# Performance work log

Measured on AMD Instinct MI355X. Metric: run time of the kernel, lower is better.

## Reference

```python
import jax, jax.numpy as jnp
import numpy as np

B, S, D, H = 2, 512, 1024, 16
HD = D // H
F, E, K = 4096, 8, 2
TEMP = 1.0
EPS = 1e-6


def setup_inputs() -> dict:
    key = jax.random.key(0)
    ks = jax.random.split(key, 12)
    sc = 0.02
    n = lambda k, shp: (jax.random.normal(k, shp, jnp.float32) * sc)
    return {
        "x": jax.random.normal(ks[0], (B, S, D), jnp.float32),
        "norm1_w": jnp.ones((D,), jnp.float32),
        "norm2_w": jnp.ones((D,), jnp.float32),
        "wq": n(ks[1], (D, D)), "bq": jnp.zeros((D,), jnp.float32),
        "wk": n(ks[2], (D, D)), "bk": jnp.zeros((D,), jnp.float32),
        "wv": n(ks[3], (D, D)), "bv": jnp.zeros((D,), jnp.float32),
        "wo": n(ks[4], (D, D)), "bo": jnp.zeros((D,), jnp.float32),
        "wr": n(ks[5], (D, E)), "br": jnp.zeros((E,), jnp.float32),
        "w1": n(ks[6], (E, D, F)), "b1": jnp.zeros((E, F), jnp.float32),
        "w2": n(ks[7], (E, F, D)), "b2": jnp.zeros((E, D), jnp.float32),
    }


def _rmsnorm(x, w):
    return x * jax.lax.rsqrt(jnp.mean(x * x, axis=-1, keepdims=True) + EPS) * w


def reference(x, norm1_w, norm2_w, wq, bq, wk, bk, wv, bv, wo, bo,
              wr, br, w1, b1, w2, b2):
    # ---- pre-norm causal multi-head attention ----
    h = _rmsnorm(x, norm1_w)
    q = (h @ wq + bq).reshape(B, S, H, HD)
    k = (h @ wk + bk).reshape(B, S, H, HD)
    v = (h @ wv + bv).reshape(B, S, H, HD)
    scores = jnp.einsum("bqhd,bkhd->bhqk", q, k) / jnp.sqrt(jnp.float32(HD))
    causal = jnp.tril(jnp.ones((S, S), bool))
    scores = jnp.where(causal, scores, jnp.finfo(scores.dtype).min)
    attn = jax.nn.softmax(scores, axis=-1)
    ctx = jnp.einsum("bhqk,bkhd->bqhd", attn, v).reshape(B, S, D)
    x = x + (ctx @ wo + bo)  # residual (dropout inert, p=0)

    # ---- temperature-scaled top-k MoE FFN ----
    h2 = _rmsnorm(x, norm2_w)
    logits = h2 @ wr + br                         # [B,S,E]
    probs = jax.nn.softmax(logits / TEMP, axis=-1)
    top_p, top_i = jax.lax.top_k(probs, K)        # [B,S,K]
    top_p = top_p / jnp.sum(top_p, axis=-1, keepdims=True)
    onehot = jax.nn.one_hot(top_i, E, dtype=probs.dtype)  # [B,S,K,E]
    combine = jnp.einsum("bsk,bske->bse", top_p, onehot)  # sparse combine weights

    # dense grouped-expert compute (reference form of dispatch/compute/combine)
    hid = jax.nn.silu(jnp.einsum("bsd,edf->bsef", h2, w1) + b1)
    expert_out = jnp.einsum("bsef,efd->bsed", hid, w2) + b2
    ff = jnp.einsum("bse,bsed->bsd", combine, expert_out)

    # load-balancing auxiliary loss: E * sum_i frac_i * mean_prob_i
    frac = jnp.mean(jnp.sum(onehot, axis=2), axis=(0, 1)) / K  # [E]
    mean_prob = jnp.mean(probs, axis=(0, 1))                   # [E]
    aux_loss = jnp.float32(E) * jnp.sum(frac * mean_prob)

    x = x + ff
    return x, aux_loss
```

## Files before the change

### kernel.cpp

```cpp
#include <hip/hip_runtime.h>
#include <math.h>

#define CB 2
#define CS 512
#define CD 1024
#define CH 16
#define CHD 64
#define CF 4096
#define CE 8
#define CK 2
#define CT (CB*CS)
#define CBH (CB*CH)
#define CEPS 1e-6f
#define QKVP 3072
#define MAXROWS 3072
#define MAXTILES (MAXROWS/128)

typedef __attribute__((ext_vector_type(8))) short bf16x8;
typedef __attribute__((ext_vector_type(4))) float f32x4;

__device__ __forceinline__ short f2bf(float f) {
  unsigned u = __float_as_uint(f);
  unsigned r = (u + 0x7FFF + ((u >> 16) & 1)) >> 16;
  return (short)r;
}
__device__ __forceinline__ float bf2f(short h) {
  return __uint_as_float(((unsigned)(unsigned short)h) << 16);
}

__device__ __forceinline__ void gload_lds16(const void* g, void* l) {
  __builtin_amdgcn_global_load_lds(
      (const __attribute__((address_space(1))) unsigned int*)g,
      (__attribute__((address_space(3))) unsigned int*)l, 16, 0, 0);
}

__global__ __launch_bounds__(256) void rmsnorm_hl_kernel(
    const float* __restrict__ x, const float* __restrict__ w,
    short* __restrict__ outH, short* __restrict__ outL) {
  int t = blockIdx.x;
  int tid = threadIdx.x;
  float4 xv = ((const float4*)(x + (size_t)t * CD))[tid];
  float ss = xv.x*xv.x + xv.y*xv.y + xv.z*xv.z + xv.w*xv.w;
  for (int off = 32; off > 0; off >>= 1) ss += __shfl_down(ss, off);
  __shared__ float red[4];
  __shared__ float s_scale;
  int lane = tid & 63, wid = tid >> 6;
  if (lane == 0) red[wid] = ss;
  __syncthreads();
  if (tid == 0) {
    float tot = red[0] + red[1] + red[2] + red[3];
    s_scale = rsqrtf(tot / (float)CD + CEPS);
  }
  __syncthreads();
  float sc = s_scale;
  float4 wv = ((const float4*)w)[tid];
  float o[4] = {xv.x * sc * wv.x, xv.y * sc * wv.y,
                xv.z * sc * wv.z, xv.w * sc * wv.w};
  short4 hi, lo;
  short* hp = (short*)&hi; short* lp = (short*)&lo;
#pragma unroll
  for (int i = 0; i < 4; ++i) {
    short h = f2bf(o[i]);
    hp[i] = h;
    lp[i] = f2bf(o[i] - bf2f(h));
  }
  ((short4*)(outH + (size_t)t * CD))[tid] = hi;
  ((short4*)(outL + (size_t)t * CD))[tid] = lo;
}

__global__ __launch_bounds__(256) void transpose_convert_kernel(
    const float* __restrict__ W, short* __restrict__ Wth,
    short* __restrict__ Wtl, int Kd, int Nd) {
  int e = blockIdx.z;
  const float* Wb = W + (size_t)e * Kd * Nd;
  size_t obase = (size_t)e * Kd * Nd;
  int n0 = blockIdx.x * 64, k0 = blockIdx.y * 64;
  __shared__ float t[64][65];
  int tid = threadIdx.x;
#pragma unroll
  for (int i = 0; i < 4; ++i) {
    int idx = i * 256 + tid;
    int r = idx >> 4, c4 = (idx & 15) * 4;
    float4 v = *(const float4*)(Wb + (size_t)(k0 + r) * Nd + n0 + c4);
    t[r][c4] = v.x; t[r][c4 + 1] = v.y; t[r][c4 + 2] = v.z; t[r][c4 + 3] = v.w;
  }
  __syncthreads();
  int n = tid >> 2, k16 = (tid & 3) * 16;
  short th[16], tl[16];
#pragma unroll
  for (int j = 0; j < 16; ++j) {
    float v = t[k16 + j][n];
    short hi = f2bf(v);
    th[j] = hi;
    tl[j] = f2bf(v - bf2f(hi));
  }
  size_t oo = obase + (size_t)(n0 + n) * Kd + k0 + k16;
  ((int4*)(Wth + oo))[0] = ((int4*)th)[0];
  ((int4*)(Wth + oo + 8))[0] = ((int4*)th)[1];
  if (Wtl) {
    ((int4*)(Wtl + oo))[0] = ((int4*)tl)[0];
    ((int4*)(Wtl + oo + 8))[0] = ((int4*)tl)[1];
  }
}

struct TPtrs {
  const float* w[4];
  short* hh[4];
  short* ll[4];
};
__global__ __launch_bounds__(256) void transpose4_kernel(TPtrs p) {
  int z = blockIdx.z;
  const float* Wb = p.w[z];
  short* Wth = p.hh[z];
  short* Wtl = p.ll[z];
  int n0 = blockIdx.x * 64, k0 = blockIdx.y * 64;
  __shared__ float t[64][65];
  int tid = threadIdx.x;
#pragma unroll
  for (int i = 0; i < 4; ++i) {
    int idx = i * 256 + tid;
    int r = idx >> 4, c4 = (idx & 15) * 4;
    float4 v = *(const float4*)(Wb + (size_t)(k0 + r) * CD + n0 + c4);
    t[r][c4] = v.x; t[r][c4 + 1] = v.y; t[r][c4 + 2] = v.z; t[r][c4 + 3] = v.w;
  }
  __syncthreads();
  int n = tid >> 2, k16 = (tid & 3) * 16;
  short th[16], tl[16];
#pragma unroll
  for (int j = 0; j < 16; ++j) {
    float v = t[k16 + j][n];
    short hi = f2bf(v);
    th[j] = hi;
    tl[j] = f2bf(v - bf2f(hi));
  }
  size_t oo = (size_t)(n0 + n) * CD + k0 + k16;
  ((int4*)(Wth + oo))[0] = ((int4*)th)[0];
  ((int4*)(Wth + oo + 8))[0] = ((int4*)th)[1];
  ((int4*)(Wtl + oo))[0] = ((int4*)tl)[0];
  ((int4*)(Wtl + oo + 8))[0] = ((int4*)tl)[1];
}

__global__ void pack_bias_kernel(const float* __restrict__ bq,
                                 const float* __restrict__ bk,
                                 const float* __restrict__ bv,
                                 float* __restrict__ out) {
  int i = blockIdx.x * 256 + threadIdx.x;
  if (i < QKVP)
    out[i] = (i < 1024) ? bq[i] : (i < 2048 ? bk[i - 1024] : bv[i - 2048]);
}

template <int SILU, int OUTBF>
__global__ __launch_bounds__(512) void moe_gemm_kernel(
    const short* __restrict__ A, const short* __restrict__ Bt,
    const float* __restrict__ bias, void* __restrict__ Cout,
    float* __restrict__ part, int partM, int N, int K,
    const int* __restrict__ tile_e, const int* __restrict__ total_rows) {
  __shared__ __align__(16) short A0[128 * 64], A1[128 * 64];
  __shared__ __align__(16) short B0[256 * 64], B1[256 * 64];
  int tid = threadIdx.x;
  int m0 = blockIdx.y * 128, n0 = blockIdx.x * 256;
  if (m0 >= *total_rows) return;
  int e = tile_e[blockIdx.y];
  const short* Bb = Bt + (size_t)e * N * K;
  const float* biasb = bias ? bias + (size_t)e * N : nullptr;
  int kz = blockIdx.z;
  int kchunk = K / gridDim.z;
  int kbeg = kz * kchunk;
  int nsteps = kchunk >> 6;
  int lane = tid & 63, w = tid >> 6;
  int wr = w >> 2, wc = w & 3;
  int l15 = lane & 15, l4 = lane >> 4;
  f32x4 acc[4][4] = {};

#define STAGE(AS_, BS_, KK)                                                   \
  {                                                                           \
    _Pragma("unroll") for (int i = 0; i < 2; ++i) {                           \
      int c = i * 512 + tid;                                                  \
      int r = c >> 3, gs = c & 7;                                             \
      int g = gs ^ (r & 7);                                                   \
      gload_lds16(A + (size_t)(m0 + r) * K + (KK) + g * 8, &AS_[c * 8]);      \
    }                                                                         \
    _Pragma("unroll") for (int i = 0; i < 4; ++i) {                           \
      int c = i * 512 + tid;                                                  \
      int r = c >> 3, gs = c & 7;                                             \
      int g = gs ^ (r & 7);                                                   \
      gload_lds16(Bb + (size_t)(n0 + r) * K + (KK) + g * 8, &BS_[c * 8]);     \
    }                                                                         \
  }

#define COMPUTE(AS_, BS_)                                                     \
  {                                                                           \
    _Pragma("unroll") for (int ks = 0; ks < 2; ++ks) {                        \
      bf16x8 a[4], b[4];                                                      \
      _Pragma("unroll") for (int m = 0; m < 4; ++m) {                         \
        int row = wr * 64 + m * 16 + l15;                                     \
        int slot = (ks * 4 + l4) ^ (row & 7);                                 \
        a[m] = *(const bf16x8*)&AS_[(row * 8 + slot) * 8];                    \
      }                                                                       \
      _Pragma("unroll") for (int n = 0; n < 4; ++n) {                         \
        int row = wc * 64 + n * 16 + l15;                                     \
        int slot = (ks * 4 + l4) ^ (row & 7);                                 \
        b[n] = *(const bf16x8*)&BS_[(row * 8 + slot) * 8];                    \
      }                                                                       \
      _Pragma("unroll") for (int m = 0; m < 4; ++m)                           \
      _Pragma("unroll") for (int n = 0; n < 4; ++n)                           \
        acc[m][n] = __builtin_amdgcn_mfma_f32_16x16x32_bf16(a[m], b[n],       \
                                                            acc[m][n], 0, 0, 0); \
    }                                                                         \
  }

  STAGE(A0, B0, kbeg);
  __syncthreads();
  for (int s = 0; s < nsteps; s += 2) {
    int k0 = kbeg + (s << 6);
    bool has1 = (s + 1 < nsteps), has2 = (s + 2 < nsteps);
    if (has1) STAGE(A1, B1, k0 + 64);
    COMPUTE(A0, B0);
    __syncthreads();
    if (has1) {
      if (has2) STAGE(A0, B0, k0 + 128);
      COMPUTE(A1, B1);
      __syncthreads();
    }
  }
#undef STAGE
#undef COMPUTE

  if (gridDim.z > 1) {
#pragma unroll
    for (int m = 0; m < 4; ++m) {
      int row = m0 + wr * 64 + m * 16 + l4 * 4;
#pragma unroll
      for (int n = 0; n < 4; ++n) {
        int col = n0 + wc * 64 + n * 16 + l15;
#pragma unroll
        for (int q = 0; q < 4; ++q)
          part[((size_t)kz * partM + row + q) * N + col] = acc[m][n][q];
      }
    }
    return;
  }
  float* outf = (float*)Cout;
  short* outb = (short*)Cout;
#pragma unroll
  for (int m = 0; m < 4; ++m) {
    int row = m0 + wr * 64 + m * 16 + l4 * 4;
#pragma unroll
    for (int n = 0; n < 4; ++n) {
      int col = n0 + wc * 64 + n * 16 + l15;
      float bv = biasb[col];
#pragma unroll
      for (int q = 0; q < 4; ++q) {
        float v = acc[m][n][q] + bv;
        if (SILU) v = v / (1.f + __expf(-v));
        if (OUTBF) outb[(size_t)(row + q) * N + col] = f2bf(v);
        else outf[(size_t)(row + q) * N + col] = v;
      }
    }
  }
}

template <int LO>
__global__ __launch_bounds__(256) void mfma_gemm_kernel(
    const short* __restrict__ Ah, const short* __restrict__ Al,
    const short* __restrict__ Bh, const short* __restrict__ Bl,
    float* __restrict__ part, int partM, int N, int K) {
  __shared__ short As0[4096], Bs0[4096], As1[4096], Bs1[4096];
  __shared__ short Als0[LO ? 4096 : 64], Bls0[LO ? 4096 : 64];
  __shared__ short Als1[LO ? 4096 : 64], Bls1[LO ? 4096 : 64];
  int tid = threadIdx.x;
  int m0 = blockIdx.y * 128, n0 = blockIdx.x * 128;
  int kz = blockIdx.z;
  int kchunk = K / gridDim.z;
  int kbeg = kz * kchunk;
  int nsteps = kchunk >> 5;
  int lane = tid & 63, w = tid >> 6;
  int wr = w >> 1, wc = w & 1;
  int l15 = lane & 15, l4 = lane >> 4;
  int xorl = (l15 & 3) ^ ((l15 >> 2) & 3);
  f32x4 acc[4][4] = {};
  bf16x8 vA0[2], vB0[2], vAl0[2], vBl0[2];
  bf16x8 vA1[2], vB1[2], vAl1[2], vBl1[2];

#define LOAD_SET(VA, VB, VAL, VBL, KK)                                        \
  {                                                                           \
    _Pragma("unroll") for (int ic = 0; ic < 2; ++ic) {                        \
      int c = ic * 256 + tid;                                                 \
      int r = c >> 2, g = c & 3;                                              \
      size_t ao = (size_t)(m0 + r) * K + (KK) + g * 8;                        \
      size_t bo = (size_t)(n0 + r) * K + (KK) + g * 8;                        \
      VA[ic] = *(const bf16x8*)(Ah + ao);                                     \
      VB[ic] = *(const bf16x8*)(Bh + bo);                                     \
      if (LO) {                                                               \
        VAL[ic] = *(const bf16x8*)(Al + ao);                                  \
        VBL[ic] = *(const bf16x8*)(Bl + bo);                                  \
      }                                                                       \
    }                                                                         \
  }

#define WRITE_SET(AS_, BS_, ALS_, BLS_, VA, VB, VAL, VBL)                     \
  {                                                                           \
    _Pragma("unroll") for (int ic = 0; ic < 2; ++ic) {                        \
      int c = ic * 256 + tid;                                                 \
      int r = c >> 2, g = c & 3;                                              \
      int ch = (r * 4 + (g ^ (r & 3) ^ ((r >> 2) & 3))) * 8;                  \
      *(bf16x8*)&AS_[ch] = VA[ic];                                            \
      *(bf16x8*)&BS_[ch] = VB[ic];                                            \
      if (LO) {                                                               \
        *(bf16x8*)&ALS_[ch] = VAL[ic];                                        \
        *(bf16x8*)&BLS_[ch] = VBL[ic];                                        \
      }                                                                       \
    }                                                                         \
  }

#define COMPUTE_SET(AS_, BS_, ALS_, BLS_)                                     \
  {                                                                           \
    bf16x8 ah[4], al[4];                                                      \
    _Pragma("unroll") for (int m = 0; m < 4; ++m) {                           \
      int row = wr * 64 + m * 16 + l15;                                       \
      int idx = (row * 4 + (l4 ^ xorl)) * 8;                                  \
      ah[m] = *(const bf16x8*)&AS_[idx];                                      \
      if (LO) al[m] = *(const bf16x8*)&ALS_[idx];                             \
    }                                                                         \
    _Pragma("unroll") for (int n = 0; n < 4; ++n) {                           \
      int row = wc * 64 + n * 16 + l15;                                       \
      int idx = (row * 4 + (l4 ^ xorl)) * 8;                                  \
      bf16x8 bhn = *(const bf16x8*)&BS_[idx];                                 \
      bf16x8 bln;                                                             \
      if (LO) bln = *(const bf16x8*)&BLS_[idx];                               \
      _Pragma("unroll") for (int m = 0; m < 4; ++m) {                         \
        acc[m][n] = __builtin_amdgcn_mfma_f32_16x16x32_bf16(ah[m], bhn,       \
                                                            acc[m][n], 0, 0, 0); \
        if (LO) {                                                             \
          acc[m][n] = __builtin_amdgcn_mfma_f32_16x16x32_bf16(al[m], bhn,     \
                                                              acc[m][n], 0, 0, 0); \
          acc[m][n] = __builtin_amdgcn_mfma_f32_16x16x32_bf16(ah[m], bln,     \
                                                              acc[m][n], 0, 0, 0); \
        }                                                                     \
      }                                                                       \
    }                                                                         \
  }

  LOAD_SET(vA0, vB0, vAl0, vBl0, kbeg);
  WRITE_SET(As0, Bs0, Als0, Bls0, vA0, vB0, vAl0, vBl0);
  __syncthreads();
  for (int s = 0; s < nsteps; s += 2) {
    int k0 = kbeg + (s << 5);
    bool has1 = (s + 1 < nsteps), has2 = (s + 2 < nsteps);
    if (has1) LOAD_SET(vA1, vB1, vAl1, vBl1, k0 + 32);
    COMPUTE_SET(As0, Bs0, Als0, Bls0);
    if (has1) WRITE_SET(As1, Bs1, Als1, Bls1, vA1, vB1, vAl1, vBl1);
    __syncthreads();
    if (has1) {
      if (has2) LOAD_SET(vA0, vB0, vAl0, vBl0, k0 + 64);
      COMPUTE_SET(As1, Bs1, Als1, Bls1);
      if (has2) WRITE_SET(As0, Bs0, Als0, Bls0, vA0, vB0, vAl0, vBl0);
      __syncthreads();
    }
  }
#undef LOAD_SET
#undef WRITE_SET
#undef COMPUTE_SET

#pragma unroll
  for (int m = 0; m < 4; ++m) {
    int row = m0 + wr * 64 + m * 16 + l4 * 4;
#pragma unroll
    for (int n = 0; n < 4; ++n) {
      int col = n0 + wc * 64 + n * 16 + l15;
#pragma unroll
      for (int q = 0; q < 4; ++q)
        part[((size_t)kz * partM + row + q) * N + col] = acc[m][n][q];
    }
  }
}

__global__ __launch_bounds__(256) void reduce_splitk_kernel(
    const float* __restrict__ part, int partM, int nz,
    const float* __restrict__ bias, float* __restrict__ outp, int N) {
  int row = blockIdx.x;
  for (int c = threadIdx.x * 4; c < N; c += 1024) {
    float4 s = *(const float4*)(part + (size_t)row * N + c);
    for (int z = 1; z < nz; ++z) {
      float4 p = *(const float4*)(part + ((size_t)z * partM + row) * N + c);
      s.x += p.x; s.y += p.y; s.z += p.z; s.w += p.w;
    }
    s.x += bias[c]; s.y += bias[c + 1]; s.z += bias[c + 2]; s.w += bias[c + 3];
    *(float4*)(outp + (size_t)row * N + c) = s;
  }
}

__global__ __launch_bounds__(256) void attn_epilogue_kernel(
    const float* __restrict__ part, const float* __restrict__ bo,
    const float* __restrict__ x, const float* __restrict__ n2w,
    const float* __restrict__ wr, const float* __restrict__ br,
    float* __restrict__ x1, float* __restrict__ h2, int* __restrict__ top_i,
    float* __restrict__ top_p, float* __restrict__ probs_out) {
  int t = blockIdx.x;
  int tid = threadIdx.x;
  int c = tid * 4;
  float4 s = *(const float4*)(part + (size_t)t * CD + c);
#pragma unroll
  for (int z = 1; z < 4; ++z) {
    float4 p = *(const float4*)(part + ((size_t)z * CT + t) * CD + c);
    s.x += p.x; s.y += p.y; s.z += p.z; s.w += p.w;
  }
  float4 bv = *(const float4*)(bo + c);
  float4 xv = *(const float4*)(x + (size_t)t * CD + c);
  s.x += bv.x + xv.x; s.y += bv.y + xv.y;
  s.z += bv.z + xv.z; s.w += bv.w + xv.w;
  *(float4*)(x1 + (size_t)t * CD + c) = s;
  float ss = s.x*s.x + s.y*s.y + s.z*s.z + s.w*s.w;
  for (int off = 32; off > 0; off >>= 1) ss += __shfl_down(ss, off);
  __shared__ float red[4];
  __shared__ float s_scale;
  int lane = tid & 63, wid = tid >> 6;
  if (lane == 0) red[wid] = ss;
  __syncthreads();
  if (tid == 0) {
    float tot = red[0] + red[1] + red[2] + red[3];
    s_scale = rsqrtf(tot / (float)CD + CEPS);
  }
  __syncthreads();
  float sc = s_scale;
  float4 wv = *(const float4*)(n2w + c);
  float hv[4] = {s.x * sc * wv.x, s.y * sc * wv.y,
                 s.z * sc * wv.z, s.w * sc * wv.w};
  *(float4*)(h2 + (size_t)t * CD + c) =
      make_float4(hv[0], hv[1], hv[2], hv[3]);
  float a[CE] = {};
#pragma unroll
  for (int j = 0; j < 4; ++j) {
    const float* wrow = wr + (size_t)(c + j) * CE;
#pragma unroll
    for (int e = 0; e < CE; ++e) a[e] += hv[j] * wrow[e];
  }
  __shared__ float red8[256][CE];
#pragma unroll
  for (int e = 0; e < CE; ++e) red8[tid][e] = a[e];
  __syncthreads();
  for (int st = 128; st > 0; st >>= 1) {
    if (tid < st) {
#pragma unroll
      for (int e = 0; e < CE; ++e) red8[tid][e] += red8[tid + st][e];
    }
    __syncthreads();
  }
  if (tid == 0) {
    float probs[CE];
    float mx = -1e30f;
#pragma unroll
    for (int e = 0; e < CE; ++e) {
      probs[e] = red8[0][e] + br[e];
      mx = fmaxf(mx, probs[e]);
    }
    float sum = 0.f;
#pragma unroll
    for (int e = 0; e < CE; ++e) { probs[e] = __expf(probs[e] - mx); sum += probs[e]; }
    float inv = 1.0f / sum;
#pragma unroll
    for (int e = 0; e < CE; ++e) {
      probs[e] *= inv;
      probs_out[t * CE + e] = probs[e];
    }
    int i1 = 0;
#pragma unroll
    for (int e = 1; e < CE; ++e) if (probs[e] > probs[i1]) i1 = e;
    int i2 = (i1 == 0) ? 1 : 0;
#pragma unroll
    for (int e = 0; e < CE; ++e)
      if (e != i1 && probs[e] > probs[i2]) i2 = e;
    float p1 = probs[i1], p2 = probs[i2];
    float s12 = p1 + p2;
    top_i[t * 2 + 0] = i1;
    top_i[t * 2 + 1] = i2;
    top_p[t * 2 + 0] = p1 / s12;
    top_p[t * 2 + 1] = p2 / s12;
  }
}

__global__ __launch_bounds__(256) void fused_attn_kernel(
    const float* __restrict__ qkv, short* __restrict__ ctxh,
    short* __restrict__ ctxl) {
  __shared__ float Qs[32][68];
  __shared__ float KVs[64 * 68];
  __shared__ float Pt[32][66];
  int qt = blockIdx.x, bh = blockIdx.y;
  int b = bh / CH, h = bh % CH;
  int qrow0 = qt * 32;
  int ktmax = (qrow0 + 31) >> 6;
  int tid = threadIdx.x;
  int cg = tid & 31, rg = tid >> 5;
  int r0 = rg * 4;

#pragma unroll
  for (int it = 0; it < 2; ++it) {
    int idx = it * 256 + tid;
    int r = idx >> 4, c4 = (idx & 15) * 4;
    *(float4*)&Qs[r][c4] = *(const float4*)(
        qkv + (size_t)(b * CS + qrow0 + r) * QKVP + h * CHD + c4);
  }

  float m_i[4], l_i[4], O[4][2];
#pragma unroll
  for (int i = 0; i < 4; ++i) {
    m_i[i] = -1e30f;
    l_i[i] = 0.f;
    O[i][0] = 0.f;
    O[i][1] = 0.f;
  }

  for (int kt = 0; kt <= ktmax; ++kt) {
    __syncthreads();
#pragma unroll
    for (int it = 0; it < 4; ++it) {
      int idx = it * 256 + tid;
      int r = idx >> 4, c4 = (idx & 15) * 4;
      const float* src =
          qkv + (size_t)(b * CS + kt * 64 + r) * QKVP + h * CHD;
      float4 kv = *(const float4*)(src + 1024 + c4);
      KVs[r * 65 + c4 + 0] = kv.x;
      KVs[r * 65 + c4 + 1] = kv.y;
      KVs[r * 65 + c4 + 2] = kv.z;
      KVs[r * 65 + c4 + 3] = kv.w;
    }
    __syncthreads();

    float s[4][2] = {};
#pragma unroll 4
    for (int d = 0; d < 64; ++d) {
      float q0 = Qs[r0 + 0][d];
      float q1 = Qs[r0 + 1][d];
      float q2 = Qs[r0 + 2][d];
      float q3 = Qs[r0 + 3][d];
      float k0 = KVs[(cg * 2 + 0) * 65 + d];
      float k1 = KVs[(cg * 2 + 1) * 65 + d];
      s[0][0] += q0 * k0; s[0][1] += q0 * k1;
      s[1][0] += q1 * k0; s[1][1] += q1 * k1;
      s[2][0] += q2 * k0; s[2][1] += q2 * k1;
      s[3][0] += q3 * k0; s[3][1] += q3 * k1;
    }

#pragma unroll
    for (int i = 0; i < 4; ++i) {
      int gr = qrow0 + r0 + i;
      int gc0 = kt * 64 + cg * 2;
      float s0 = (gc0 + 0 > gr) ? -1e30f : s[i][0] * 0.125f;
      float s1 = (gc0 + 1 > gr) ? -1e30f : s[i][1] * 0.125f;
      float tmax = fmaxf(s0, s1);
#pragma unroll
      for (int off = 16; off > 0; off >>= 1)
        tmax = fmaxf(tmax, __shfl_xor(tmax, off));
      float newm = fmaxf(m_i[i], tmax);
      float p0 = __expf(s0 - newm);
      float p1 = __expf(s1 - newm);
      float tsum = p0 + p1;
#pragma unroll
      for (int off = 16; off > 0; off >>= 1) tsum += __shfl_xor(tsum, off);
      float scale = __expf(m_i[i] - newm);
      l_i[i] = l_i[i] * scale + tsum;
      m_i[i] = newm;
      O[i][0] *= scale;
      O[i][1] *= scale;
      Pt[r0 + i][cg * 2 + 0] = p0;
      Pt[r0 + i][cg * 2 + 1] = p1;
    }
    __syncthreads();

#pragma unroll
    for (int it = 0; it < 4; ++it) {
      int idx = it * 256 + tid;
      int r = idx >> 4, c4 = (idx & 15) * 4;
      *(float4*)&KVs[r * 68 + c4] = *(const float4*)(
          qkv + (size_t)(b * CS + kt * 64 + r) * QKVP + 2048 + h * CHD + c4);
    }
    __syncthreads();

#pragma unroll 4
    for (int c = 0; c < 64; ++c) {
      float p0 = Pt[r0 + 0][c];
      float p1 = Pt[r0 + 1][c];
      float p2 = Pt[r0 + 2][c];
      float p3 = Pt[r0 + 3][c];
      float v0 = KVs[c * 68 + cg];
      float v1 = KVs[c * 68 + cg + 32];
      O[0][0] += p0 * v0; O[0][1] += p0 * v1;
      O[1][0] += p1 * v0; O[1][1] += p1 * v1;
      O[2][0] += p2 * v0; O[2][1] += p2 * v1;
      O[3][0] += p3 * v0; O[3][1] += p3 * v1;
    }
  }

#pragma unroll
  for (int i = 0; i < 4; ++i) {
    float inv = 1.0f / l_i[i];
#pragma unroll
    for (int jd = 0; jd < 2; ++jd) {
      int dv = cg + 32 * jd;
      size_t oi = (size_t)(b * CS + qrow0 + r0 + i) * CD + h * CHD + dv;
      float v = O[i][jd] * inv;
      short hi = f2bf(v);
      ctxh[oi] = hi;
      ctxl[oi] = f2bf(v - bf2f(hi));
    }
  }
}

__global__ __launch_bounds__(256) void finalize_kernel(
    const int* __restrict__ top_i, const float* __restrict__ probs,
    int* __restrict__ offs, int* __restrict__ tile_e,
    int* __restrict__ total_padded, int* __restrict__ row_map,
    int* __restrict__ cursor, float* __restrict__ aux_out) {
  int tid = threadIdx.x;
  __shared__ float redp[256][CE];
  __shared__ int redc[256][CE];
  float lp[CE] = {};
  int lc[CE] = {};
  for (int t = tid; t < CT; t += 256) {
    lc[top_i[t * 2 + 0]]++;
    lc[top_i[t * 2 + 1]]++;
#pragma unroll
    for (int e = 0; e < CE; ++e) lp[e] += probs[t * CE + e];
  }
#pragma unroll
  for (int e = 0; e < CE; ++e) { redp[tid][e] = lp[e]; redc[tid][e] = lc[e]; }
  __syncthreads();
  for (int s = 128; s > 0; s >>= 1) {
    if (tid < s) {
#pragma unroll
      for (int e = 0; e < CE; ++e) {
        redp[tid][e] += redp[tid + s][e];
        redc[tid][e] += redc[tid + s][e];
      }
    }
    __syncthreads();
  }
  __shared__ int s_off[CE + 1];
  if (tid == 0) {
    int o = 0;
    for (int e = 0; e < CE; ++e) {
      s_off[e] = o;
      offs[e] = o;
      o += ((redc[0][e] + 127) >> 7) << 7;
    }
    s_off[CE] = o;
    offs[CE] = o;
    *total_padded = o;
    int nt = o >> 7;
    for (int i = 0; i < nt; ++i) {
      int e = 0;
      while (e < CE - 1 && i * 128 >= s_off[e + 1]) e++;
      tile_e[i] = e;
    }
    float aux = 0.f;
    for (int e = 0; e < CE; ++e)
      aux += ((float)redc[0][e] / (float)(CT * CK)) * (redp[0][e] / (float)CT);
    aux_out[0] = aux * (float)CE;
  }
  if (tid < CE) cursor[tid] = 0;
  __syncthreads();
  for (int i = tid; i < MAXROWS; i += blockDim.x) row_map[i] = -1;
}

__global__ void gather_kernel(const int* __restrict__ top_i,
                              const int* __restrict__ offs,
                              int* __restrict__ cursor, int* __restrict__ row_map,
                              int* __restrict__ row_of) {
  int idx = blockIdx.x * blockDim.x + threadIdx.x;
  if (idx >= CT * CK) return;
  int e = top_i[idx];
  int pos = offs[e] + atomicAdd(&cursor[e], 1);
  row_map[pos] = idx >> 1;
  row_of[idx] = pos;
}

__global__ __launch_bounds__(256) void gatherx_kernel(
    const float* __restrict__ h2, const int* __restrict__ row_map,
    short* __restrict__ Xg) {
  int row = blockIdx.x;
  int tid = threadIdx.x;
  int tok = row_map[row];
  short4 o;
  if (tok < 0) {
    o = make_short4(0, 0, 0, 0);
  } else {
    float4 v = ((const float4*)(h2 + (size_t)tok * CD))[tid];
    o = make_short4(f2bf(v.x), f2bf(v.y), f2bf(v.z), f2bf(v.w));
  }
  ((short4*)(Xg + (size_t)row * CD))[tid] = o;
}

__global__ __launch_bounds__(256) void combine_g2_kernel(
    const float* __restrict__ part, int partM, int nz,
    const float* __restrict__ b2, const int* __restrict__ tile_e,
    const int* __restrict__ row_of, const float* __restrict__ top_p,
    const float* __restrict__ x1, float* __restrict__ out) {
  int t = blockIdx.x;
  int c = threadIdx.x * 4;
  float4 r = *(const float4*)(x1 + (size_t)t * CD + c);
#pragma unroll
  for (int s = 0; s < CK; ++s) {
    int row = row_of[t * 2 + s];
    int e = tile_e[row >> 7];
    float w = top_p[t * 2 + s];
    float4 acc = *(const float4*)(part + (size_t)row * CD + c);
    for (int z = 1; z < nz; ++z) {
      float4 p = *(const float4*)(part + ((size_t)z * partM + row) * CD + c);
      acc.x += p.x; acc.y += p.y; acc.z += p.z; acc.w += p.w;
    }
    float4 bv = *(const float4*)(b2 + (size_t)e * CD + c);
    r.x += w * (acc.x + bv.x);
    r.y += w * (acc.y + bv.y);
    r.z += w * (acc.z + bv.z);
    r.w += w * (acc.w + bv.w);
  }
  *(float4*)(out + (size_t)t * CD + c) = r;
}

extern "C" void kernel_launch(void* const* d_in, const int* in_sizes, int n_in,
                              void* d_out, int out_size, void* d_ws,
                              size_t ws_size, hipStream_t stream) {
  const float* x   = (const float*)d_in[0];
  const float* n1w = (const float*)d_in[1];
  const float* n2w = (const float*)d_in[2];
  const float* wq  = (const float*)d_in[3];
  const float* bq  = (const float*)d_in[4];
  const float* wk  = (const float*)d_in[5];
  const float* bk  = (const float*)d_in[6];
  const float* wv  = (const float*)d_in[7];
  const float* bv  = (const float*)d_in[8];
  const float* wo  = (const float*)d_in[9];
  const float* bo  = (const float*)d_in[10];
  const float* wr  = (const float*)d_in[11];
  const float* br  = (const float*)d_in[12];
  const float* w1  = (const float*)d_in[13];
  const float* b1  = (const float*)d_in[14];
  const float* w2  = (const float*)d_in[15];
  const float* b2  = (const float*)d_in[16];
  float* out = (float*)d_out;

  char* base = (char*)d_ws;
  size_t off = 0;
  auto alloc = [&](size_t bytes) -> void* {
    void* p = base + off;
    off += (bytes + 255) & ~(size_t)255;
    return p;
  };
  float* f_x1   = (float*)alloc((size_t)CT * CD * 4);
  float* f_h2   = (float*)alloc((size_t)CT * CD * 4);
  short* f_xg   = (short*)alloc((size_t)MAXROWS * CD * 2);
  short* f_hid  = (short*)alloc((size_t)MAXROWS * CF * 2);
  short* f_hh   = (short*)alloc((size_t)CT * CD * 2);
  short* f_hl   = (short*)alloc((size_t)CT * CD * 2);
  short* f_wqkvh = (short*)alloc((size_t)QKVP * CD * 2);
  short* f_wqkvl = (short*)alloc((size_t)QKVP * CD * 2);
  float* f_qkv  = (float*)alloc((size_t)CT * QKVP * 4);
  short* f_ctxh = (short*)alloc((size_t)CT * CD * 2);
  short* f_ctxl = (short*)alloc((size_t)CT * CD * 2);
  short* f_woth = (short*)alloc((size_t)CD * CD * 2);
  short* f_wotl = (short*)alloc((size_t)CD * CD * 2);
  float* f_bqkv = (float*)alloc(QKVP * 4);
  float* f_topp = (float*)alloc(CT * CK * 4);
  float* f_probs = (float*)alloc(CT * CE * 4);
  int* i_topi   = (int*)alloc(CT * CK * 4);
  int* i_rowof  = (int*)alloc(CT * CK * 4);
  int* i_rowmap = (int*)alloc(MAXROWS * 4);
  int* i_cursor = (int*)alloc(CE * 4);
  int* i_offs   = (int*)alloc((CE + 1) * 4);
  int* i_tile   = (int*)alloc(MAXTILES * 4);
  int* i_total  = (int*)alloc(4);
  short* f_wG = (short*)alloc((size_t)CE * CD * CF * 2);
  short* f_w1t = f_wG;
  short* f_w2t = f_wG;
  void* Rs = alloc((size_t)4 * MAXROWS * CD * 4);
  float* f_partqkv = (float*)Rs;
  float* f_partwo = (float*)Rs;
  float* f_partg2 = (float*)Rs;

  dim3 b256(256);

  pack_bias_kernel<<<QKVP / 256, b256, 0, stream>>>(bq, bk, bv, f_bqkv);
  TPtrs tp;
  tp.w[0] = wq; tp.w[1] = wk; tp.w[2] = wv; tp.w[3] = wo;
  tp.hh[0] = f_wqkvh + 0 * (size_t)CD * CD;
  tp.hh[1] = f_wqkvh + 1 * (size_t)CD * CD;
  tp.hh[2] = f_wqkvh + 2 * (size_t)CD * CD;
  tp.hh[3] = f_woth;
  tp.ll[0] = f_wqkvl + 0 * (size_t)CD * CD;
  tp.ll[1] = f_wqkvl + 1 * (size_t)CD * CD;
  tp.ll[2] = f_wqkvl + 2 * (size_t)CD * CD;
  tp.ll[3] = f_wotl;
  transpose4_kernel<<<dim3(16, 16, 4), b256, 0, stream>>>(tp);
  transpose_convert_kernel<<<dim3(CF / 64, CD / 64, CE), b256, 0, stream>>>(
      w1, f_w1t, nullptr, CD, CF);

  rmsnorm_hl_kernel<<<CT, b256, 0, stream>>>(x, n1w, f_hh, f_hl);
  mfma_gemm_kernel<1><<<dim3(QKVP / 128, CT / 128, 2), b256, 0, stream>>>(
      f_hh, f_hl, f_wqkvh, f_wqkvl, f_partqkv, CT, QKVP, CD);
  reduce_splitk_kernel<<<CT, b256, 0, stream>>>(f_partqkv, CT, 2, f_bqkv,
                                                f_qkv, QKVP);
  fused_attn_kernel<<<dim3(CS / 32, CBH), b256, 0, stream>>>(f_qkv, f_ctxh,
                                                             f_ctxl);
  mfma_gemm_kernel<1><<<dim3(CD / 128, CT / 128, 4), b256, 0, stream>>>(
      f_ctxh, f_ctxl, f_woth, f_wotl, f_partwo, CT, CD, CD);
  attn_epilogue_kernel<<<CT, b256, 0, stream>>>(f_partwo, bo, x, n2w, wr, br,
                                                f_x1, f_h2, i_topi, f_topp,
                                                f_probs);

  finalize_kernel<<<1, 256, 0, stream>>>(i_topi, f_probs, i_offs, i_tile,
                                         i_total, i_rowmap, i_cursor,
                                         out + (size_t)CT * CD);
  gather_kernel<<<(CT * CK + 255) / 256, b256, 0, stream>>>(i_topi, i_offs,
                                                            i_cursor, i_rowmap,
                                                            i_rowof);
  gatherx_kernel<<<MAXROWS, b256, 0, stream>>>(f_h2, i_rowmap, f_xg);

  moe_gemm_kernel<1, 1><<<dim3(CF / 256, MAXTILES, 1), dim3(512), 0, stream>>>(
      f_xg, f_w1t, b1, f_hid, nullptr, 0, CF, CD, i_tile, i_total);
  transpose_convert_kernel<<<dim3(CD / 64, CF / 64, CE), b256, 0, stream>>>(
      w2, f_w2t, nullptr, CF, CD);
  moe_gemm_kernel<0, 0><<<dim3(CD / 256, MAXTILES, 4), dim3(512), 0, stream>>>(
      f_hid, f_w2t, nullptr, nullptr, f_partg2, MAXROWS, CD, CF, i_tile,
      i_total);
  combine_g2_kernel<<<CT, b256, 0, stream>>>(f_partg2, MAXROWS, 4, b2, i_tile,
                                             i_rowof, f_topp, f_x1, out);
}
```

Baseline: 351.6 us.

## Drop split-K for QKV GEMM with fused bias epilogue; vectorize attention P loads

The QKV projection GEMM now runs without split-K and adds the bias directly in its epilogue, writing the final qkv buffer. This removes the partial-sum buffer round trip and the separate reduction kernel launch, at the cost of fewer blocks (192 instead of 384) and longer per-block K loops. The attention kernel also pads the P tile to 68 columns and uses float2 stores and float4 loads for P in the PV loop, cutting the number of LDS instructions.

Result: faster. 343.6 us (-2.3%).

```diff
diff --git a/kernel.cpp b/kernel.cpp
--- a/kernel.cpp
+++ b/kernel.cpp
@@ -264,6 +264,7 @@
 __global__ __launch_bounds__(256) void mfma_gemm_kernel(
     const short* __restrict__ Ah, const short* __restrict__ Al,
     const short* __restrict__ Bh, const short* __restrict__ Bl,
+    const float* __restrict__ bias, float* __restrict__ dout,
     float* __restrict__ part, int partM, int N, int K) {
   __shared__ short As0[4096], Bs0[4096], As1[4096], Bs1[4096];
   __shared__ short Als0[LO ? 4096 : 64], Bls0[LO ? 4096 : 64];
@@ -362,31 +363,31 @@
 #undef WRITE_SET
 #undef COMPUTE_SET
 
+  if (gridDim.z > 1) {
+#pragma unroll
+    for (int m = 0; m < 4; ++m) {
+      int row = m0 + wr * 64 + m * 16 + l4 * 4;
+#pragma unroll
+      for (int n = 0; n < 4; ++n) {
+        int col = n0 + wc * 64 + n * 16 + l15;
+#pragma unroll
+        for (int q = 0; q < 4; ++q)
+          part[((size_t)kz * partM + row + q) * N + col] = acc[m][n][q];
+      }
+    }
+    return;
+  }
 #pragma unroll
   for (int m = 0; m < 4; ++m) {
     int row = m0 + wr * 64 + m * 16 + l4 * 4;
 #pragma unroll
     for (int n = 0; n < 4; ++n) {
       int col = n0 + wc * 64 + n * 16 + l15;
+      float bv = bias[col];
 #pragma unroll
       for (int q = 0; q < 4; ++q)
-        part[((size_t)kz * partM + row + q) * N + col] = acc[m][n][q];
-    }
-  }
-}
-
-__global__ __launch_bounds__(256) void reduce_splitk_kernel(
-    const float* __restrict__ part, int partM, int nz,
-    const float* __restrict__ bias, float* __restrict__ outp, int N) {
-  int row = blockIdx.x;
-  for (int c = threadIdx.x * 4; c < N; c += 1024) {
-    float4 s = *(const float4*)(part + (size_t)row * N + c);
-    for (int z = 1; z < nz; ++z) {
-      float4 p = *(const float4*)(part + ((size_t)z * partM + row) * N + c);
-      s.x += p.x; s.y += p.y; s.z += p.z; s.w += p.w;
-    }
-    s.x += bias[c]; s.y += bias[c + 1]; s.z += bias[c + 2]; s.w += bias[c + 3];
-    *(float4*)(outp + (size_t)row * N + c) = s;
+        dout[(size_t)(row + q) * N + col] = acc[m][n][q] + bv;
+    }
   }
 }
 
@@ -484,7 +485,7 @@
     short* __restrict__ ctxl) {
   __shared__ float Qs[32][68];
   __shared__ float KVs[64 * 68];
-  __shared__ float Pt[32][66];
+  __shared__ float Pt[32][68];
   int qt = blockIdx.x, bh = blockIdx.y;
   int b = bh / CH, h = bh % CH;
   int qrow0 = qt * 32;
@@ -562,8 +563,7 @@
       m_i[i] = newm;
       O[i][0] *= scale;
       O[i][1] *= scale;
-      Pt[r0 + i][cg * 2 + 0] = p0;
-      Pt[r0 + i][cg * 2 + 1] = p1;
+      *(float2*)&Pt[r0 + i][cg * 2] = make_float2(p0, p1);
     }
     __syncthreads();
 
@@ -576,18 +576,25 @@
     }
     __syncthreads();
 
-#pragma unroll 4
-    for (int c = 0; c < 64; ++c) {
-      float p0 = Pt[r0 + 0][c];
-      float p1 = Pt[r0 + 1][c];
-      float p2 = Pt[r0 + 2][c];
-      float p3 = Pt[r0 + 3][c];
-      float v0 = KVs[c * 68 + cg];
-      float v1 = KVs[c * 68 + cg + 32];
-      O[0][0] += p0 * v0; O[0][1] += p0 * v1;
-      O[1][0] += p1 * v0; O[1][1] += p1 * v1;
-      O[2][0] += p2 * v0; O[2][1] += p2 * v1;
-      O[3][0] += p3 * v0; O[3][1] += p3 * v1;
+#pragma unroll 2
+    for (int c4 = 0; c4 < 64; c4 += 4) {
+      float4 pr[4];
+#pragma unroll
+      for (int i = 0; i < 4; ++i) pr[i] = *(const float4*)&Pt[r0 + i][c4];
+      float pv[4][4] = {{pr[0].x, pr[0].y, pr[0].z, pr[0].w},
+                        {pr[1].x, pr[1].y, pr[1].z, pr[1].w},
+                        {pr[2].x, pr[2].y, pr[2].z, pr[2].w},
+                        {pr[3].x, pr[3].y, pr[3].z, pr[3].w}};
+#pragma unroll
+      for (int j = 0; j < 4; ++j) {
+        int c = c4 + j;
+        float v0 = KVs[c * 68 + cg];
+        float v1 = KVs[c * 68 + cg + 32];
+        O[0][0] += pv[0][j] * v0; O[0][1] += pv[0][j] * v1;
+        O[1][0] += pv[1][j] * v0; O[1][1] += pv[1][j] * v1;
+        O[2][0] += pv[2][j] * v0; O[2][1] += pv[2][j] * v1;
+        O[3][0] += pv[3][j] * v0; O[3][1] += pv[3][j] * v1;
+      }
     }
   }
 
@@ -773,7 +780,6 @@
   short* f_w1t = f_wG;
   short* f_w2t = f_wG;
   void* Rs = alloc((size_t)4 * MAXROWS * CD * 4);
-  float* f_partqkv = (float*)Rs;
   float* f_partwo = (float*)Rs;
   float* f_partg2 = (float*)Rs;
 
@@ -795,14 +801,12 @@
       w1, f_w1t, nullptr, CD, CF);
 
   rmsnorm_hl_kernel<<<CT, b256, 0, stream>>>(x, n1w, f_hh, f_hl);
-  mfma_gemm_kernel<1><<<dim3(QKVP / 128, CT / 128, 2), b256, 0, stream>>>(
-      f_hh, f_hl, f_wqkvh, f_wqkvl, f_partqkv, CT, QKVP, CD);
-  reduce_splitk_kernel<<<CT, b256, 0, stream>>>(f_partqkv, CT, 2, f_bqkv,
-                                                f_qkv, QKVP);
+  mfma_gemm_kernel<1><<<dim3(QKVP / 128, CT / 128, 1), b256, 0, stream>>>(
+      f_hh, f_hl, f_wqkvh, f_wqkvl, f_bqkv, f_qkv, nullptr, CT, QKVP, CD);
   fused_attn_kernel<<<dim3(CS / 32, CBH), b256, 0, stream>>>(f_qkv, f_ctxh,
                                                              f_ctxl);
   mfma_gemm_kernel<1><<<dim3(CD / 128, CT / 128, 4), b256, 0, stream>>>(
-      f_ctxh, f_ctxl, f_woth, f_wotl, f_partwo, CT, CD, CD);
+      f_ctxh, f_ctxl, f_woth, f_wotl, nullptr, nullptr, f_partwo, CT, CD, CD);
   attn_epilogue_kernel<<<CT, b256, 0, stream>>>(f_partwo, bo, x, n2w, wr, br,
                                                 f_x1, f_h2, i_topi, f_topp,
                                                 f_probs);
```
